# Kernel optimization log

Hardware: AMD Instinct MI355X
Metric: run time of the kernel (lower is better)

Reference implementation:

```python
import jax, jax.numpy as jnp
import numpy as np

EMBED_DIM = 512


def setup_inputs() -> dict:
    key = jax.random.key(0)
    k1, k2, k3 = jax.random.split(key, 3)
    B, T, E = 8, 2048, EMBED_DIM
    x = jax.random.normal(k1, (B, T, E), dtype=jnp.float32)
    # Linear weights stored [in, out] (torch stores [out, in]; math is identical via transpose)
    Wq = jax.random.normal(k2, (E, E), dtype=jnp.float32) * (E ** -0.5)
    bq = jnp.zeros((E,), dtype=jnp.float32)
    Wk = jax.random.normal(k3, (E, E), dtype=jnp.float32) * (E ** -0.5)
    bk = jnp.zeros((E,), dtype=jnp.float32)
    return {"x": x, "Wq": Wq, "bq": bq, "Wk": Wk, "bk": bk}


def reference(x, Wq, bq, Wk, bk) -> jnp.ndarray:
    scaling = jnp.float32(EMBED_DIM ** -0.5)
    q = (x @ Wq + bq) * scaling          # [B, T, E]
    k = x @ Wk + bk                       # [B, T, E]
    scores = jnp.einsum("bqe,bke->bqk", q, k)   # [B, T, T]
    attn = jax.nn.softmax(scores, axis=-1)
    return jnp.einsum("bqk,bke->bqe", attn, x)  # V = x
```

## Files before the change

kernel.cpp:

```cpp
#include <hip/hip_runtime.h>
#include <hip/hip_bf16.h>
#include <stdint.h>

#define B_  8
#define T_  2048
#define E_  512

typedef __attribute__((ext_vector_type(8))) __bf16 bf16x8;
typedef __attribute__((ext_vector_type(8))) unsigned short ushort8;
typedef __attribute__((ext_vector_type(4))) unsigned short ushort4v;
typedef __attribute__((ext_vector_type(4))) float f32x4;

__device__ __forceinline__ float bf2f(unsigned short u) {
  union { unsigned int u; float f; } c; c.u = ((unsigned int)u) << 16; return c.f;
}
__device__ __forceinline__ unsigned short f2bf(float f) {
  union { float f; unsigned int u; } c; c.f = f;
  unsigned int u = c.u;
  unsigned int r = (u + 0x7FFFu + ((u >> 16) & 1u)) >> 16;
  return (unsigned short)r;
}

__device__ __forceinline__ void gload_lds16(const void* g, void* l) {
  __builtin_amdgcn_global_load_lds(
      (const __attribute__((address_space(1))) uint32_t*)g,
      (__attribute__((address_space(3))) uint32_t*)l, 16, 0, 0);
}

__global__ __launch_bounds__(256)
void trans_conv_kernel(const float* __restrict__ x, unsigned short* __restrict__ xbf,
                       unsigned short* __restrict__ xT) {
  __shared__ unsigned short tile[64][66];
  const int t0 = blockIdx.x * 64, e0 = blockIdx.y * 64, b = blockIdx.z;
  const int tid = threadIdx.x;
  const float* xb = x + ((size_t)b * T_ + t0) * E_ + e0;
  unsigned short* xbf_b = xbf + ((size_t)b * T_ + t0) * E_ + e0;
#pragma unroll
  for (int it = 0; it < 4; ++it) {
    int tr = (tid >> 4) + it * 16;
    int ec = (tid & 15) * 4;
    float4 f = *reinterpret_cast<const float4*>(xb + (size_t)tr * E_ + ec);
    ushort4v o;
    o[0] = f2bf(f.x); o[1] = f2bf(f.y); o[2] = f2bf(f.z); o[3] = f2bf(f.w);
    *reinterpret_cast<ushort4v*>(xbf_b + (size_t)tr * E_ + ec) = o;
    tile[ec + 0][tr] = o[0];
    tile[ec + 1][tr] = o[1];
    tile[ec + 2][tr] = o[2];
    tile[ec + 3][tr] = o[3];
  }
  __syncthreads();
  unsigned short* dst = xT + ((size_t)b * E_ + e0) * T_ + t0;
#pragma unroll
  for (int it = 0; it < 2; ++it) {
    int er = (tid >> 3) + it * 32;
    int tg = (tid & 7) * 8;
    ushort8 r;
#pragma unroll
    for (int j = 0; j < 8; ++j) r[j] = tile[er][tg + j];
    *reinterpret_cast<ushort8*>(dst + (size_t)er * T_ + tg) = r;
  }
}

__global__ __launch_bounds__(256)
void conv_w_kernel(const float* __restrict__ Wq, const float* __restrict__ Wk,
                   const float* __restrict__ bq, const float* __restrict__ bk,
                   unsigned short* __restrict__ WT, float* __restrict__ bqk, float scale) {
  int idx = blockIdx.x * 256 + threadIdx.x;
  int n  = idx >> 9;
  int kk = idx & 511;
  float v = (n < E_) ? Wq[kk * E_ + n] * scale : Wk[kk * E_ + (n - E_)];
  WT[idx] = f2bf(v);
  if (idx < 2 * E_) {
    float bv = (idx < E_) ? bq[idx] * scale : bk[idx - E_];
    bqk[idx] = bv;
  }
}

#define STG_A1(abuf_, kt) do {                                                  \
  _Pragma("unroll") for (int r_ = 0; r_ < 4; ++r_)                              \
    gload_lds16(gA + (long long)(r_ * 32) * lda + (long long)(kt) * 64,         \
                &sm[(abuf_) * 8192 + r_ * 2048 + tid * 8]);                     \
} while (0)

#define STG_B1(bbuf_, kt) do {                                                  \
  _Pragma("unroll") for (int r_ = 0; r_ < 4; ++r_)                              \
    gload_lds16(gB + (long long)(r_ * 32) * ldb + (long long)(kt) * 64,         \
                &sm[24576 + (bbuf_) * 8192 + r_ * 2048 + tid * 8]);             \
} while (0)

template<int OUT>
__global__ __launch_bounds__(256)
void gemm1b(const unsigned short* __restrict__ A, int lda, long long strA,
            const unsigned short* __restrict__ B, int ldb, long long strB,
            void* __restrict__ Cv, int ldc, long long strC,
            int K, const float* __restrict__ bias, int NBX, int NBY,
            float* __restrict__ Rg, const float* __restrict__ invR)
{
  __shared__ unsigned short sm[40960];
  const int tid  = threadIdx.x;
  const int lane = tid & 63;
  const int wv   = tid >> 6;
  const int wrp  = wv >> 1;
  const int wcp  = wv & 1;
  const int fr   = lane & 15;

  const int nwg = gridDim.x, bid = blockIdx.x;
  const int qq = nwg >> 3, rr = nwg & 7, xc = bid & 7, ii = bid >> 3;
  const int wg = (xc < rr ? xc * (qq + 1) : rr * (qq + 1) + (xc - rr) * qq) + ii;
  const int bx = wg % NBX;
  const int tt = wg / NBX;
  const int by = tt % NBY;
  const int bz = tt / NBY;

  const long long m0 = (long long)by * 128;
  const long long n0 = (long long)bx * 128;
  const unsigned short* Ab = A + (long long)bz * strA + m0 * lda;
  const unsigned short* Bb = B + (long long)bz * strB + n0 * ldb;

  const int srow = tid >> 3;
  const int scol = ((tid & 7) * 8) ^ ((srow & 7) << 3);
  const unsigned short* gA = Ab + (long long)srow * lda + scol;
  const unsigned short* gB = Bb + (long long)srow * ldb + scol;

  const int xorc  = (fr & 7) << 3;
  const int q8    = (lane >> 4) * 8;
  const int c0    = q8 ^ xorc;
  const int c1    = (32 + q8) ^ xorc;
  const int aRow  = (wrp * 64 + fr) * 64;
  const int bRow  = (wcp * 64 + fr) * 64;

  f32x4 acc[4][4];
#pragma unroll
  for (int i = 0; i < 4; ++i)
#pragma unroll
    for (int j = 0; j < 4; ++j) acc[i][j] = (f32x4){0.f, 0.f, 0.f, 0.f};

  bf16x8 aA[4][2], bB4[4][2];
  const int NT = K >> 6;

  STG_A1(0, 0);
  STG_B1(0, 0);
  STG_A1(1, 1);
  asm volatile("s_waitcnt vmcnt(4)" ::: "memory");
  __builtin_amdgcn_s_barrier();

  int ab = 0;
  int bb = 0;
  for (int t = 0; t < NT; ++t) {
    if (t + 1 < NT) STG_B1(bb ^ 1, t + 1);
    if (t + 2 < NT) { int ab2 = ab + 2; if (ab2 >= 3) ab2 -= 3; STG_A1(ab2, t + 2); }
    const int pbA = ab * 8192;
    const int pbB = 24576 + bb * 8192;
#pragma unroll
    for (int m = 0; m < 4; ++m) {
      aA[m][0] = *reinterpret_cast<const bf16x8*>(&sm[pbA + aRow + m * 1024 + c0]);
      aA[m][1] = *reinterpret_cast<const bf16x8*>(&sm[pbA + aRow + m * 1024 + c1]);
    }
#pragma unroll
    for (int n = 0; n < 4; ++n) {
      bB4[n][0] = *reinterpret_cast<const bf16x8*>(&sm[pbB + bRow + n * 1024 + c0]);
      bB4[n][1] = *reinterpret_cast<const bf16x8*>(&sm[pbB + bRow + n * 1024 + c1]);
    }
    __builtin_amdgcn_s_setprio(1);
#pragma unroll
    for (int m = 0; m < 4; ++m)
#pragma unroll
      for (int n = 0; n < 4; ++n) {
        acc[m][n] = __builtin_amdgcn_mfma_f32_16x16x32_bf16(aA[m][0], bB4[n][0], acc[m][n], 0, 0, 0);
        acc[m][n] = __builtin_amdgcn_mfma_f32_16x16x32_bf16(aA[m][1], bB4[n][1], acc[m][n], 0, 0, 0);
      }
    __builtin_amdgcn_s_setprio(0);
    if (t + 2 < NT)      asm volatile("s_waitcnt vmcnt(4)" ::: "memory");
    else                 asm volatile("s_waitcnt vmcnt(0)" ::: "memory");
    __builtin_amdgcn_s_barrier();
    ab = (ab == 2) ? 0 : ab + 1;
    bb ^= 1;
  }

  const int rq = (lane >> 4) * 4;
  if (OUT == 2) {
    float* Cb = (float*)Cv + (long long)bz * strC;
#pragma unroll
    for (int m = 0; m < 4; ++m)
#pragma unroll
      for (int j = 0; j < 4; ++j) {
        const int lrow = wrp * 64 + m * 16 + rq + j;
        const long long row = m0 + lrow;
        const float inv = invR[bz * 2048 + row];
#pragma unroll
        for (int n = 0; n < 4; ++n)
          Cb[row * ldc + n0 + wcp * 64 + n * 16 + fr] = acc[m][n][j] * inv;
      }
    return;
  }
  if (OUT == 1) {
#pragma unroll
    for (int m = 0; m < 4; ++m)
#pragma unroll
      for (int n = 0; n < 4; ++n)
#pragma unroll
        for (int j = 0; j < 4; ++j) acc[m][n][j] = __expf(acc[m][n][j]);
    float* rps = (float*)(sm + 17664);
#pragma unroll
    for (int m = 0; m < 4; ++m)
#pragma unroll
      for (int j = 0; j < 4; ++j) {
        float s = acc[m][0][j] + acc[m][1][j] + acc[m][2][j] + acc[m][3][j];
        s += __shfl_xor(s, 1); s += __shfl_xor(s, 2);
        s += __shfl_xor(s, 4); s += __shfl_xor(s, 8);
        if (fr == 0) rps[wcp * 128 + wrp * 64 + m * 16 + rq + j] = s;
      }
  } else if (bias) {
#pragma unroll
    for (int n = 0; n < 4; ++n) {
      const float bv = bias[n0 + wcp * 64 + n * 16 + fr];
#pragma unroll
      for (int m = 0; m < 4; ++m)
#pragma unroll
        for (int j = 0; j < 4; ++j) acc[m][n][j] += bv;
    }
  }
#pragma unroll
  for (int m = 0; m < 4; ++m)
#pragma unroll
    for (int j = 0; j < 4; ++j) {
      const int lrow = wrp * 64 + m * 16 + rq + j;
#pragma unroll
      for (int n = 0; n < 4; ++n)
        sm[lrow * 136 + wcp * 64 + n * 16 + fr] = f2bf(acc[m][n][j]);
    }
  __syncthreads();
  if (OUT == 1) {
    float* rps = (float*)(sm + 17664);
    if (tid < 128) {
      const float s = rps[tid] + rps[128 + tid];
      Rg[((long long)bz * NBX + bx) * 2048 + m0 + tid] = s;
    }
  }
  unsigned short* C = (unsigned short*)Cv + (long long)bz * strC;
#pragma unroll
  for (int it = 0; it < 8; ++it) {
    const int row = it * 16 + (tid >> 4);
    const int chunk = tid & 15;
    ushort8 v = *reinterpret_cast<const ushort8*>(&sm[row * 136 + chunk * 8]);
    *reinterpret_cast<ushort8*>(&C[(m0 + row) * ldc + n0 + chunk * 8]) = v;
  }
}

__global__ __launch_bounds__(256)
void rowsum_inv_kernel(const float* __restrict__ R, float* __restrict__ invR) {
  const int i = blockIdx.x * 256 + threadIdx.x;
  const int b = i >> 11, t = i & 2047;
  float s = 0.f;
#pragma unroll
  for (int c = 0; c < 16; ++c) s += R[((long long)(b * 16 + c)) * 2048 + t];
  invR[i] = 1.0f / s;
}

extern "C" void kernel_launch(void* const* d_in, const int* in_sizes, int n_in,
                              void* d_out, int out_size, void* d_ws, size_t ws_size,
                              hipStream_t stream)
{
  const float* x  = (const float*)d_in[0];
  const float* Wq = (const float*)d_in[1];
  const float* bq = (const float*)d_in[2];
  const float* Wk = (const float*)d_in[3];
  const float* bk = (const float*)d_in[4];
  float* out = (float*)d_out;

  char* w = (char*)d_ws;
  unsigned short* xbf  = (unsigned short*)w;  w += (size_t)B_ * T_ * E_ * 2;
  unsigned short* xT   = (unsigned short*)w;  w += (size_t)B_ * T_ * E_ * 2;
  unsigned short* WT   = (unsigned short*)w;  w += (size_t)2 * E_ * E_ * 2;
  float*          bqk  = (float*)w;           w += (size_t)2 * E_ * 4;
  float*          R    = (float*)w;           w += (size_t)B_ * 16 * T_ * 4;
  float*          invR = (float*)w;           w += (size_t)B_ * T_ * 4;
  unsigned short* qk   = (unsigned short*)w;  w += (size_t)B_ * T_ * 2 * E_ * 2;
  unsigned short* attn = (unsigned short*)w;  w += (size_t)B_ * T_ * T_ * 2;

  const float scale = 0.044194173824159216f;

  trans_conv_kernel<<<dim3(32, 8, 8), 256, 0, stream>>>(x, xbf, xT);
  conv_w_kernel<<<2048, 256, 0, stream>>>(Wq, Wk, bq, bk, WT, bqk, scale);

  gemm1b<0><<<1024, 256, 0, stream>>>(
      xbf, E_, 0, WT, E_, 0, qk, 2 * E_, 0, E_, bqk, 8, 128, nullptr, nullptr);

  gemm1b<1><<<2048, 256, 0, stream>>>(
      qk, 2 * E_, (long long)T_ * 2 * E_,
      qk + E_, 2 * E_, (long long)T_ * 2 * E_,
      attn, T_, (long long)T_ * T_, E_, nullptr, 16, 16, R, nullptr);

  rowsum_inv_kernel<<<64, 256, 0, stream>>>(R, invR);

  gemm1b<2><<<512, 256, 0, stream>>>(
      attn, T_, (long long)T_ * T_,
      xT, T_, (long long)E_ * T_,
      out, E_, (long long)T_ * E_, T_, nullptr, 4, 16, nullptr, invR);
}
```

Measured before the change: 142.5 us.

## Switch GEMMs to 32x32x16 MFMA and fold row-sum inverse into final GEMM

Replaces the 16x16x32 bf16 MFMA tiling with 32x32x16 MFMA tiles, giving 2x2 accumulators of 16 floats per wave. The LDS fragment addressing, softmax row-sum shuffles and epilogue row mapping are rewritten to match. The separate rowsum_inv kernel is removed, and each block of the final GEMM now reduces the partial row sums itself before writing the output. The larger MFMA issues fewer instructions per K step. The cost is that partial-sum reduction work is repeated across the column blocks of the last GEMM.

```diff
diff --git a/kernel.cpp b/kernel.cpp
--- a/kernel.cpp
+++ b/kernel.cpp
@@ -9,7 +9,7 @@
 typedef __attribute__((ext_vector_type(8))) __bf16 bf16x8;
 typedef __attribute__((ext_vector_type(8))) unsigned short ushort8;
 typedef __attribute__((ext_vector_type(4))) unsigned short ushort4v;
-typedef __attribute__((ext_vector_type(4))) float f32x4;
+typedef __attribute__((ext_vector_type(16))) float f32x16;
 
 __device__ __forceinline__ float bf2f(unsigned short u) {
   union { unsigned int u; float f; } c; c.u = ((unsigned int)u) << 16; return c.f;
@@ -90,11 +90,11 @@
 
 template<int OUT>
 __global__ __launch_bounds__(256)
-void gemm1b(const unsigned short* __restrict__ A, int lda, long long strA,
+void gemm32(const unsigned short* __restrict__ A, int lda, long long strA,
             const unsigned short* __restrict__ B, int ldb, long long strB,
             void* __restrict__ Cv, int ldc, long long strC,
             int K, const float* __restrict__ bias, int NBX, int NBY,
-            float* __restrict__ Rg, const float* __restrict__ invR)
+            float* __restrict__ Rg)
 {
   __shared__ unsigned short sm[40960];
   const int tid  = threadIdx.x;
@@ -102,7 +102,10 @@
   const int wv   = tid >> 6;
   const int wrp  = wv >> 1;
   const int wcp  = wv & 1;
-  const int fr   = lane & 15;
+  const int l31  = lane & 31;
+  const int h8   = (lane >> 5) * 8;
+  const int h4   = (lane >> 5) * 4;
+  const int xorc = (lane & 7) << 3;
 
   const int nwg = gridDim.x, bid = blockIdx.x;
   const int qq = nwg >> 3, rr = nwg & 7, xc = bid & 7, ii = bid >> 3;
@@ -122,20 +125,18 @@
   const unsigned short* gA = Ab + (long long)srow * lda + scol;
   const unsigned short* gB = Bb + (long long)srow * ldb + scol;
 
-  const int xorc  = (fr & 7) << 3;
-  const int q8    = (lane >> 4) * 8;
-  const int c0    = q8 ^ xorc;
-  const int c1    = (32 + q8) ^ xorc;
-  const int aRow  = (wrp * 64 + fr) * 64;
-  const int bRow  = (wcp * 64 + fr) * 64;
-
-  f32x4 acc[4][4];
-#pragma unroll
-  for (int i = 0; i < 4; ++i)
-#pragma unroll
-    for (int j = 0; j < 4; ++j) acc[i][j] = (f32x4){0.f, 0.f, 0.f, 0.f};
-
-  bf16x8 aA[4][2], bB4[4][2];
+  const int aBase = (wrp * 64 + l31) * 64;
+  const int bBase = (wcp * 64 + l31) * 64;
+
+  f32x16 acc[2][2];
+#pragma unroll
+  for (int i = 0; i < 2; ++i)
+#pragma unroll
+    for (int j = 0; j < 2; ++j)
+#pragma unroll
+      for (int e = 0; e < 16; ++e) acc[i][j][e] = 0.f;
+
+  bf16x8 aA[2][4], bBv[2][4];
   const int NT = K >> 6;
 
   STG_A1(0, 0);
@@ -152,23 +153,26 @@
     const int pbA = ab * 8192;
     const int pbB = 24576 + bb * 8192;
 #pragma unroll
-    for (int m = 0; m < 4; ++m) {
-      aA[m][0] = *reinterpret_cast<const bf16x8*>(&sm[pbA + aRow + m * 1024 + c0]);
-      aA[m][1] = *reinterpret_cast<const bf16x8*>(&sm[pbA + aRow + m * 1024 + c1]);
-    }
-#pragma unroll
-    for (int n = 0; n < 4; ++n) {
-      bB4[n][0] = *reinterpret_cast<const bf16x8*>(&sm[pbB + bRow + n * 1024 + c0]);
-      bB4[n][1] = *reinterpret_cast<const bf16x8*>(&sm[pbB + bRow + n * 1024 + c1]);
-    }
+    for (int mt = 0; mt < 2; ++mt)
+#pragma unroll
+      for (int ks = 0; ks < 4; ++ks)
+        aA[mt][ks] = *reinterpret_cast<const bf16x8*>(
+            &sm[pbA + aBase + mt * 2048 + ((ks * 16 + h8) ^ xorc)]);
+#pragma unroll
+    for (int nt = 0; nt < 2; ++nt)
+#pragma unroll
+      for (int ks = 0; ks < 4; ++ks)
+        bBv[nt][ks] = *reinterpret_cast<const bf16x8*>(
+            &sm[pbB + bBase + nt * 2048 + ((ks * 16 + h8) ^ xorc)]);
     __builtin_amdgcn_s_setprio(1);
 #pragma unroll
-    for (int m = 0; m < 4; ++m)
-#pragma unroll
-      for (int n = 0; n < 4; ++n) {
-        acc[m][n] = __builtin_amdgcn_mfma_f32_16x16x32_bf16(aA[m][0], bB4[n][0], acc[m][n], 0, 0, 0);
-        acc[m][n] = __builtin_amdgcn_mfma_f32_16x16x32_bf16(aA[m][1], bB4[n][1], acc[m][n], 0, 0, 0);
-      }
+    for (int mt = 0; mt < 2; ++mt)
+#pragma unroll
+      for (int nt = 0; nt < 2; ++nt)
+#pragma unroll
+        for (int ks = 0; ks < 4; ++ks)
+          acc[mt][nt] = __builtin_amdgcn_mfma_f32_32x32x16_bf16(
+              aA[mt][ks], bBv[nt][ks], acc[mt][nt], 0, 0, 0);
     __builtin_amdgcn_s_setprio(0);
     if (t + 2 < NT)      asm volatile("s_waitcnt vmcnt(4)" ::: "memory");
     else                 asm volatile("s_waitcnt vmcnt(0)" ::: "memory");
@@ -177,57 +181,69 @@
     bb ^= 1;
   }
 
-  const int rq = (lane >> 4) * 4;
   if (OUT == 2) {
+    float* rsum = (float*)sm;
+    if (tid < 128) {
+      float s = 0.f;
+#pragma unroll
+      for (int c = 0; c < 16; ++c)
+        s += Rg[((long long)(bz * 16 + c)) * 2048 + m0 + tid];
+      rsum[tid] = 1.0f / s;
+    }
+    __syncthreads();
     float* Cb = (float*)Cv + (long long)bz * strC;
 #pragma unroll
-    for (int m = 0; m < 4; ++m)
-#pragma unroll
-      for (int j = 0; j < 4; ++j) {
-        const int lrow = wrp * 64 + m * 16 + rq + j;
+    for (int mt = 0; mt < 2; ++mt)
+#pragma unroll
+      for (int reg = 0; reg < 16; ++reg) {
+        const int lrow = wrp * 64 + mt * 32 + (reg & 3) + 8 * (reg >> 2) + h4;
+        const float inv = rsum[lrow];
         const long long row = m0 + lrow;
-        const float inv = invR[bz * 2048 + row];
-#pragma unroll
-        for (int n = 0; n < 4; ++n)
-          Cb[row * ldc + n0 + wcp * 64 + n * 16 + fr] = acc[m][n][j] * inv;
+#pragma unroll
+        for (int nt = 0; nt < 2; ++nt)
+          Cb[row * ldc + n0 + wcp * 64 + nt * 32 + l31] = acc[mt][nt][reg] * inv;
       }
     return;
   }
   if (OUT == 1) {
 #pragma unroll
-    for (int m = 0; m < 4; ++m)
-#pragma unroll
-      for (int n = 0; n < 4; ++n)
-#pragma unroll
-        for (int j = 0; j < 4; ++j) acc[m][n][j] = __expf(acc[m][n][j]);
+    for (int mt = 0; mt < 2; ++mt)
+#pragma unroll
+      for (int nt = 0; nt < 2; ++nt)
+#pragma unroll
+        for (int reg = 0; reg < 16; ++reg) acc[mt][nt][reg] = __expf(acc[mt][nt][reg]);
     float* rps = (float*)(sm + 17664);
 #pragma unroll
-    for (int m = 0; m < 4; ++m)
-#pragma unroll
-      for (int j = 0; j < 4; ++j) {
-        float s = acc[m][0][j] + acc[m][1][j] + acc[m][2][j] + acc[m][3][j];
+    for (int mt = 0; mt < 2; ++mt)
+#pragma unroll
+      for (int reg = 0; reg < 16; ++reg) {
+        float s = acc[mt][0][reg] + acc[mt][1][reg];
         s += __shfl_xor(s, 1); s += __shfl_xor(s, 2);
-        s += __shfl_xor(s, 4); s += __shfl_xor(s, 8);
-        if (fr == 0) rps[wcp * 128 + wrp * 64 + m * 16 + rq + j] = s;
+        s += __shfl_xor(s, 4); s += __shfl_xor(s, 8); s += __shfl_xor(s, 16);
+        if (l31 == 0) {
+          const int lrow = wrp * 64 + mt * 32 + (reg & 3) + 8 * (reg >> 2) + h4;
+          rps[wcp * 128 + lrow] = s;
+        }
       }
   } else if (bias) {
-#pragma unroll
-    for (int n = 0; n < 4; ++n) {
-      const float bv = bias[n0 + wcp * 64 + n * 16 + fr];
-#pragma unroll
-      for (int m = 0; m < 4; ++m)
-#pragma unroll
-        for (int j = 0; j < 4; ++j) acc[m][n][j] += bv;
-    }
-  }
-#pragma unroll
-  for (int m = 0; m < 4; ++m)
-#pragma unroll
-    for (int j = 0; j < 4; ++j) {
-      const int lrow = wrp * 64 + m * 16 + rq + j;
-#pragma unroll
-      for (int n = 0; n < 4; ++n)
-        sm[lrow * 136 + wcp * 64 + n * 16 + fr] = f2bf(acc[m][n][j]);
+    float bv[2];
+#pragma unroll
+    for (int nt = 0; nt < 2; ++nt) bv[nt] = bias[n0 + wcp * 64 + nt * 32 + l31];
+#pragma unroll
+    for (int mt = 0; mt < 2; ++mt)
+#pragma unroll
+      for (int nt = 0; nt < 2; ++nt)
+#pragma unroll
+        for (int reg = 0; reg < 16; ++reg) acc[mt][nt][reg] += bv[nt];
+  }
+#pragma unroll
+  for (int mt = 0; mt < 2; ++mt)
+#pragma unroll
+    for (int reg = 0; reg < 16; ++reg) {
+      const int lrow = wrp * 64 + mt * 32 + (reg & 3) + 8 * (reg >> 2) + h4;
+#pragma unroll
+      for (int nt = 0; nt < 2; ++nt)
+        sm[lrow * 136 + wcp * 64 + nt * 32 + l31] = f2bf(acc[mt][nt][reg]);
     }
   __syncthreads();
   if (OUT == 1) {
@@ -245,16 +261,6 @@
     ushort8 v = *reinterpret_cast<const ushort8*>(&sm[row * 136 + chunk * 8]);
     *reinterpret_cast<ushort8*>(&C[(m0 + row) * ldc + n0 + chunk * 8]) = v;
   }
-}
-
-__global__ __launch_bounds__(256)
-void rowsum_inv_kernel(const float* __restrict__ R, float* __restrict__ invR) {
-  const int i = blockIdx.x * 256 + threadIdx.x;
-  const int b = i >> 11, t = i & 2047;
-  float s = 0.f;
-#pragma unroll
-  for (int c = 0; c < 16; ++c) s += R[((long long)(b * 16 + c)) * 2048 + t];
-  invR[i] = 1.0f / s;
 }
 
 extern "C" void kernel_launch(void* const* d_in, const int* in_sizes, int n_in,
@@ -274,7 +280,6 @@
   unsigned short* WT   = (unsigned short*)w;  w += (size_t)2 * E_ * E_ * 2;
   float*          bqk  = (float*)w;           w += (size_t)2 * E_ * 4;
   float*          R    = (float*)w;           w += (size_t)B_ * 16 * T_ * 4;
-  float*          invR = (float*)w;           w += (size_t)B_ * T_ * 4;
   unsigned short* qk   = (unsigned short*)w;  w += (size_t)B_ * T_ * 2 * E_ * 2;
   unsigned short* attn = (unsigned short*)w;  w += (size_t)B_ * T_ * T_ * 2;
 
@@ -283,18 +288,16 @@
   trans_conv_kernel<<<dim3(32, 8, 8), 256, 0, stream>>>(x, xbf, xT);
   conv_w_kernel<<<2048, 256, 0, stream>>>(Wq, Wk, bq, bk, WT, bqk, scale);
 
-  gemm1b<0><<<1024, 256, 0, stream>>>(
-      xbf, E_, 0, WT, E_, 0, qk, 2 * E_, 0, E_, bqk, 8, 128, nullptr, nullptr);
-
-  gemm1b<1><<<2048, 256, 0, stream>>>(
+  gemm32<0><<<1024, 256, 0, stream>>>(
+      xbf, E_, 0, WT, E_, 0, qk, 2 * E_, 0, E_, bqk, 8, 128, nullptr);
+
+  gemm32<1><<<2048, 256, 0, stream>>>(
       qk, 2 * E_, (long long)T_ * 2 * E_,
       qk + E_, 2 * E_, (long long)T_ * 2 * E_,
-      attn, T_, (long long)T_ * T_, E_, nullptr, 16, 16, R, nullptr);
-
-  rowsum_inv_kernel<<<64, 256, 0, stream>>>(R, invR);
-
-  gemm1b<2><<<512, 256, 0, stream>>>(
+      attn, T_, (long long)T_ * T_, E_, nullptr, 16, 16, R);
+
+  gemm32<2><<<512, 256, 0, stream>>>(
       attn, T_, (long long)T_ * T_,
       xT, T_, (long long)E_ * T_,
-      out, E_, (long long)T_ * E_, T_, nullptr, 4, 16, nullptr, invR);
-}
+      out, E_, (long long)T_ * E_, T_, nullptr, 4, 16, R);
+}
```

Measured after the change: 166.4 us. 1.17x slower.
